# Optimization experiments

Measured on AMD Instinct MI355X. Metric: run time of the kernel, lower is better.

The kernel has to match this reference:

```python
import jax, jax.numpy as jnp
import numpy as np

B, S, D, H = 2, 2048, 1280, 16
DEPTH = D // H  # 80


def setup_inputs() -> dict:
    key = jax.random.key(0)
    ks = jax.random.split(key, 6)
    scale = 1.0 / np.sqrt(D)
    x = jax.random.normal(ks[0], (B, S, D), dtype=jnp.float32)
    # causal mask: 1.0 where attention is disallowed (strict upper triangle)
    mask = jnp.triu(jnp.ones((S, S), dtype=jnp.float32), k=1)
    Wq = jax.random.normal(ks[1], (D, D), dtype=jnp.float32) * scale
    Wk = jax.random.normal(ks[2], (D, D), dtype=jnp.float32) * scale
    Wv = jax.random.normal(ks[3], (D, D), dtype=jnp.float32) * scale
    Wo = jax.random.normal(ks[4], (D, D), dtype=jnp.float32) * scale
    z = jnp.zeros((D,), dtype=jnp.float32)
    return {"x": x, "mask": mask, "Wq": Wq, "bq": z, "Wk": Wk, "bk": z,
            "Wv": Wv, "bv": z, "Wo": Wo, "bo": z}


def _split_heads(t):
    # [B, S, D] -> [B, H, S, depth]
    return t.reshape(B, -1, H, DEPTH).transpose(0, 2, 1, 3)


def reference(x, mask, Wq, bq, Wk, bk, Wv, bv, Wo, bo):
    q = _split_heads(x @ Wq + bq)
    k = _split_heads(x @ Wk + bk)
    v = _split_heads(x @ Wv + bv)
    # scaled dot-product attention with additive (masked * -10000) logits
    logits = jnp.einsum("bhqd,bhkd->bhqk", q, k) / jnp.sqrt(
        jnp.asarray(DEPTH, dtype=jnp.float32))
    logits = logits + mask * -10000.0  # mask broadcasts over [B, H]
    attn = jax.nn.softmax(logits, axis=-1)
    ctx = jnp.einsum("bhqk,bhkd->bhqd", attn, v)
    ctx = ctx.transpose(0, 2, 1, 3).reshape(B, -1, D)  # merge heads
    return ctx @ Wo + bo
```

## Files before the change

### kernel.cpp

```cpp
#include <hip/hip_runtime.h>

typedef unsigned short u16;
typedef __bf16 bf16;
typedef __bf16 bf16x8 __attribute__((ext_vector_type(8)));
typedef unsigned short u16x8 __attribute__((ext_vector_type(8)));
typedef float f32x4 __attribute__((ext_vector_type(4)));

constexpr int B_ = 2, S_ = 2048, D_ = 1280, H_ = 16, DEPTH_ = 80;
constexpr int M_ = B_ * S_;
constexpr int QR_ = 128;

__device__ inline u16 f2b(float f) { return __builtin_bit_cast(u16, (bf16)f); }

typedef __attribute__((address_space(1))) const void gvoid;
typedef __attribute__((address_space(3))) void lvoid;
__device__ inline void gl_lds16(const void* g, void* l) {
  __builtin_amdgcn_global_load_lds((gvoid*)g, (lvoid*)l, 16, 0, 0);
}

__global__ __launch_bounds__(256) void convx_k(const float* __restrict__ src,
                                               u16* __restrict__ dst) {
  int i0 = (blockIdx.x * 256 + threadIdx.x) * 8;
  u16x8 v;
#pragma unroll
  for (int j = 0; j < 8; ++j) v[j] = f2b(src[i0 + j]);
  *(u16x8*)(dst + i0) = v;
}

__global__ __launch_bounds__(256) void pad0_k(u16* __restrict__ QK) {
  int c = blockIdx.x * 256 + threadIdx.x;
  int r = c / 6, k = c - r * 6;
  u16x8 z = {};
  *(u16x8*)(QK + (size_t)r * QR_ + 80 + k * 8) = z;
}

__global__ __launch_bounds__(256) void transpose4_k(const float* W0, const float* W1,
                                                    const float* W2, const float* W3,
                                                    u16* __restrict__ WT) {
  const float* srcs[4] = {W0, W1, W2, W3};
  const float* W = srcs[blockIdx.z];
  u16* out = WT + (size_t)blockIdx.z * D_ * D_;
  __shared__ u16 t[32][33];
  int tx = threadIdx.x, ty = threadIdx.y;
  int x0 = blockIdx.x * 32, y0 = blockIdx.y * 32;
#pragma unroll
  for (int i = 0; i < 4; ++i)
    t[ty + 8 * i][tx] = f2b(W[(size_t)(y0 + ty + 8 * i) * D_ + x0 + tx]);
  __syncthreads();
#pragma unroll
  for (int i = 0; i < 4; ++i)
    out[(size_t)(x0 + ty + 8 * i) * D_ + y0 + tx] = t[tx][ty + 8 * i];
}

struct GemmAcc {
  f32x4 acc[4][4];
};
__device__ inline void gemm_core(const u16* __restrict__ A,
                                 const u16* __restrict__ BT, int m0, int n0,
                                 u16* a_s, u16* b_s, GemmAcc& g) {
  int tid = threadIdx.x, lane = tid & 63, wave = tid >> 6;
  int quad = lane >> 4, l15 = lane & 15;
  int wm = wave >> 1, wn = wave & 1;
  int rr8 = lane >> 3;
  int csw = ((lane & 7) ^ rr8) * 8;
  int sw15 = l15 & 7;

  for (int k0 = 0; k0 < D_; k0 += 64) {
    __syncthreads();
#pragma unroll
    for (int j = 0; j < 4; ++j) {
      int ch = wave * 4 + j;
      gl_lds16(A + (size_t)(m0 + ch * 8 + rr8) * D_ + k0 + csw, a_s + ch * 512);
      gl_lds16(BT + (size_t)(n0 + ch * 8 + rr8) * D_ + k0 + csw, b_s + ch * 512);
    }
    __syncthreads();
#pragma unroll
    for (int ks = 0; ks < 2; ++ks) {
      int pos = (((ks << 2) | quad) ^ sw15) * 8;
      bf16x8 af[4], bfr[4];
#pragma unroll
      for (int mt = 0; mt < 4; ++mt)
        af[mt] = *(const bf16x8*)(a_s + (wm * 64 + mt * 16 + l15) * 64 + pos);
#pragma unroll
      for (int nt = 0; nt < 4; ++nt)
        bfr[nt] = *(const bf16x8*)(b_s + (wn * 64 + nt * 16 + l15) * 64 + pos);
#pragma unroll
      for (int mt = 0; mt < 4; ++mt)
#pragma unroll
        for (int nt = 0; nt < 4; ++nt)
          g.acc[mt][nt] = __builtin_amdgcn_mfma_f32_16x16x32_bf16(
              af[mt], bfr[nt], g.acc[mt][nt], 0, 0, 0);
    }
  }
}

__global__ __launch_bounds__(256) void gemm_qkv(const u16* __restrict__ A,
                                                const u16* __restrict__ BT,
                                                const float* __restrict__ bq,
                                                const float* __restrict__ bk,
                                                const float* __restrict__ bv,
                                                u16* __restrict__ Qw,
                                                u16* __restrict__ Kw,
                                                u16* __restrict__ Vw) {
  __shared__ __align__(16) u16 a_s[128 * 64];
  __shared__ __align__(16) u16 b_s[128 * 64];
  int lane = threadIdx.x & 63, wave = threadIdx.x >> 6;
  int quad = lane >> 4, l15 = lane & 15;
  int wm = wave >> 1, wn = wave & 1;
  int m0 = blockIdx.y * 128, n0 = blockIdx.x * 128;

  GemmAcc g = {};
  gemm_core(A, BT, m0, n0, a_s, b_s, g);

  int mat = n0 / D_;
  const float* bp = (mat == 0) ? bq : (mat == 1 ? bk : bv);
#pragma unroll
  for (int nt = 0; nt < 4; ++nt) {
    int ng = n0 + wn * 64 + nt * 16 + l15;
    int co = ng - mat * D_;
    float bv_ = bp[co];
    int h = co / DEPTH_, d = co % DEPTH_;
#pragma unroll
    for (int mt = 0; mt < 4; ++mt)
#pragma unroll
      for (int r = 0; r < 4; ++r) {
        int row = m0 + wm * 64 + mt * 16 + quad * 4 + r;
        int b = row >> 11, s = row & (S_ - 1);
        u16 bits = f2b(g.acc[mt][nt][r] + bv_);
        if (mat < 2) {
          u16* outp = mat ? Kw : Qw;
          outp[((size_t)(b * H_ + h) * S_ + s) * QR_ + d] = bits;
        } else {
          Vw[((size_t)(b * H_ + h) * DEPTH_ + d) * S_ + s] = bits;
        }
      }
  }
}

__global__ __launch_bounds__(256) void gemm_out(const u16* __restrict__ A,
                                                const u16* __restrict__ BT,
                                                const float* __restrict__ bias,
                                                float* __restrict__ out) {
  __shared__ __align__(16) u16 a_s[128 * 64];
  __shared__ __align__(16) u16 b_s[128 * 64];
  int lane = threadIdx.x & 63, wave = threadIdx.x >> 6;
  int quad = lane >> 4, l15 = lane & 15;
  int wm = wave >> 1, wn = wave & 1;
  int m0 = blockIdx.y * 128, n0 = blockIdx.x * 128;

  GemmAcc g = {};
  gemm_core(A, BT, m0, n0, a_s, b_s, g);

#pragma unroll
  for (int nt = 0; nt < 4; ++nt) {
    int col = n0 + wn * 64 + nt * 16 + l15;
    float bv = bias[col];
#pragma unroll
    for (int mt = 0; mt < 4; ++mt)
#pragma unroll
      for (int r = 0; r < 4; ++r) {
        int row = m0 + wm * 64 + mt * 16 + quad * 4 + r;
        out[(size_t)row * D_ + col] = g.acc[mt][nt][r] + bv;
      }
  }
}

__global__ __launch_bounds__(256, 4) void attn_k(const u16* __restrict__ Qp,
                                                 const u16* __restrict__ Kp,
                                                 const u16* __restrict__ VT,
                                                 u16* __restrict__ ctx) {
  constexpr float SCALE = 0.11180339887498949f;
  __shared__ __align__(16) u16 k_s[64 * 128];
  __shared__ __align__(16) u16 vt_s[80 * 64];
  __shared__ __align__(16) u16 p_s[64 * 72];
  int tid = threadIdx.x, lane = tid & 63, wave = tid >> 6;
  int quad = lane >> 4, l15 = lane & 15;
  int bx = blockIdx.x, by = blockIdx.y;
  int s_ = (by >> 4) & 1;
  int qt = s_ ? (31 - bx) : bx;
  int bh = (by & 15) | (((by >> 5) & 1) << 4);
  const u16* Qb = Qp + (size_t)bh * S_ * QR_;
  const u16* Kb = Kp + (size_t)bh * S_ * QR_;
  const u16* Vb = VT + (size_t)bh * DEPTH_ * S_;

  bf16x8 qf[3];
#pragma unroll
  for (int ks = 0; ks < 3; ++ks)
    qf[ks] = *(const bf16x8*)(Qb + (size_t)(qt * 64 + wave * 16 + l15) * QR_ +
                              ks * 32 + quad * 8);

  f32x4 acc_o[5] = {};
  float lsum[4] = {};

  for (int kt = 0; kt <= qt; ++kt) {
    int k0 = kt * 64;
    __syncthreads();
#pragma unroll
    for (int i = 0; i < 4; ++i) {
      int row = wave * 4 + quad + 16 * i;
      int sc = l15 ^ (row & 7);
      gl_lds16(Kb + (size_t)(k0 + row) * QR_ + sc * 8,
               k_s + (size_t)row * QR_ + l15 * 8);
    }
#pragma unroll
    for (int i = 0; i < 3; ++i) {
      int ch = tid + 256 * i;
      if (ch < 640) {
        int row = ch >> 3, pos = ch & 7;
        int sc = pos ^ (row & 7);
        gl_lds16(Vb + (size_t)row * S_ + k0 + sc * 8, vt_s + ch * 8);
      }
    }
    __syncthreads();

    f32x4 sa[4] = {};
#pragma unroll
    for (int ks = 0; ks < 3; ++ks) {
      int pa = ((ks * 4 + quad) ^ (l15 & 7)) * 8;
#pragma unroll
      for (int nt = 0; nt < 4; ++nt) {
        bf16x8 bfr = *(const bf16x8*)(k_s + (size_t)(nt * 16 + l15) * QR_ + pa);
        sa[nt] = __builtin_amdgcn_mfma_f32_16x16x32_bf16(qf[ks], bfr, sa[nt], 0, 0, 0);
      }
    }
    bool diag = (kt == qt);
#pragma unroll
    for (int nt = 0; nt < 4; ++nt)
#pragma unroll
      for (int r = 0; r < 4; ++r) {
        float p = __expf(sa[nt][r] * SCALE);
        if (diag && (nt * 16 + l15) > (wave * 16 + quad * 4 + r)) p = 0.0f;
        sa[nt][r] = p;
        lsum[r] += p;
      }
    asm volatile("s_waitcnt lgkmcnt(0)" ::: "memory");
#pragma unroll
    for (int nt = 0; nt < 4; ++nt)
#pragma unroll
      for (int r = 0; r < 4; ++r)
        p_s[(wave * 16 + quad * 4 + r) * 72 + nt * 16 + l15] = f2b(sa[nt][r]);
    asm volatile("s_waitcnt lgkmcnt(0)" ::: "memory");
#pragma unroll
    for (int kk = 0; kk < 2; ++kk) {
      bf16x8 af = *(const bf16x8*)(p_s + (wave * 16 + l15) * 72 + kk * 32 + quad * 8);
#pragma unroll
      for (int d5 = 0; d5 < 5; ++d5) {
        int pv = ((kk * 4 + quad) ^ (l15 & 7)) * 8;
        bf16x8 bfr = *(const bf16x8*)(vt_s + (size_t)(d5 * 16 + l15) * 64 + pv);
        acc_o[d5] = __builtin_amdgcn_mfma_f32_16x16x32_bf16(af, bfr, acc_o[d5], 0, 0, 0);
      }
    }
  }

#pragma unroll
  for (int r = 0; r < 4; ++r)
#pragma unroll
    for (int m = 1; m < 16; m <<= 1) lsum[r] += __shfl_xor(lsum[r], m, 16);

  int b = bh >> 4, h = bh & 15;
#pragma unroll
  for (int d5 = 0; d5 < 5; ++d5)
#pragma unroll
    for (int r = 0; r < 4; ++r) {
      int s = qt * 64 + wave * 16 + quad * 4 + r;
      int col = h * DEPTH_ + d5 * 16 + l15;
      ctx[(size_t)(b * S_ + s) * D_ + col] = f2b(acc_o[d5][r] / lsum[r]);
    }
}

extern "C" void kernel_launch(void* const* d_in, const int* in_sizes, int n_in,
                              void* d_out, int out_size, void* d_ws, size_t ws_size,
                              hipStream_t stream) {
  const float* x  = (const float*)d_in[0];
  const float* Wq = (const float*)d_in[2];
  const float* bq = (const float*)d_in[3];
  const float* Wk = (const float*)d_in[4];
  const float* bk = (const float*)d_in[5];
  const float* Wv = (const float*)d_in[6];
  const float* bv = (const float*)d_in[7];
  const float* Wo = (const float*)d_in[8];
  const float* bo = (const float*)d_in[9];

  const size_t DD = (size_t)D_ * D_;
  const size_t QE = (size_t)B_ * H_ * S_ * DEPTH_;
  const size_t QP = (size_t)B_ * H_ * S_ * QR_;
  u16* xbf = (u16*)d_ws;
  u16* wT  = xbf + QE;
  u16* Qw  = wT + 4 * DD;
  u16* Kw  = Qw + QP;
  u16* Vw  = Kw + QP;
  u16* Cw  = xbf;
  size_t need = (size_t)(Vw + QE - xbf) * 2;
  if (ws_size < need) return;

  convx_k<<<(int)(QE / 2048), 256, 0, stream>>>(x, xbf);
  pad0_k<<<3072, 256, 0, stream>>>(Qw);
  transpose4_k<<<dim3(D_ / 32, D_ / 32, 4), dim3(32, 8), 0, stream>>>(Wq, Wk, Wv,
                                                                      Wo, wT);
  gemm_qkv<<<dim3(3 * D_ / 128, M_ / 128), 256, 0, stream>>>(xbf, wT, bq, bk, bv,
                                                             Qw, Kw, Vw);
  attn_k<<<dim3(16, 64), 256, 0, stream>>>(Qw, Kw, Vw, Cw);
  gemm_out<<<dim3(D_ / 128, M_ / 128), 256, 0, stream>>>(Cw, wT + 3 * DD, bo,
                                                         (float*)d_out);
}
```

Baseline: 276.1 us.

## Merge prep kernels into one launch and shrink GEMM K-tile to 32

Folds the x conversion, Q/K padding zeroing and the four weight transposes into a single prep kernel, cutting two launches. The shared GEMM core moves from a 64-wide K tile with XOR-swizzled LDS to a 32-wide unswizzled tile, halving LDS per block. Launch bounds are raised to 4 blocks per CU to allow higher occupancy. The price is twice as many barrier-separated K iterations and possible LDS bank conflicts from dropping the swizzle.

```diff
diff --git a/kernel.cpp b/kernel.cpp
--- a/kernel.cpp
+++ b/kernel.cpp
@@ -18,38 +18,43 @@
   __builtin_amdgcn_global_load_lds((gvoid*)g, (lvoid*)l, 16, 0, 0);
 }
 
-__global__ __launch_bounds__(256) void convx_k(const float* __restrict__ src,
-                                               u16* __restrict__ dst) {
-  int i0 = (blockIdx.x * 256 + threadIdx.x) * 8;
-  u16x8 v;
-#pragma unroll
-  for (int j = 0; j < 8; ++j) v[j] = f2b(src[i0 + j]);
-  *(u16x8*)(dst + i0) = v;
-}
-
-__global__ __launch_bounds__(256) void pad0_k(u16* __restrict__ QK) {
-  int c = blockIdx.x * 256 + threadIdx.x;
-  int r = c / 6, k = c - r * 6;
-  u16x8 z = {};
-  *(u16x8*)(QK + (size_t)r * QR_ + 80 + k * 8) = z;
-}
-
-__global__ __launch_bounds__(256) void transpose4_k(const float* W0, const float* W1,
-                                                    const float* W2, const float* W3,
-                                                    u16* __restrict__ WT) {
-  const float* srcs[4] = {W0, W1, W2, W3};
-  const float* W = srcs[blockIdx.z];
-  u16* out = WT + (size_t)blockIdx.z * D_ * D_;
+__global__ __launch_bounds__(256) void prep_k(const float* __restrict__ x,
+                                              u16* __restrict__ xbf,
+                                              u16* __restrict__ QK,
+                                              const float* __restrict__ W0,
+                                              const float* __restrict__ W1,
+                                              const float* __restrict__ W2,
+                                              const float* __restrict__ W3,
+                                              u16* __restrict__ WT) {
   __shared__ u16 t[32][33];
-  int tx = threadIdx.x, ty = threadIdx.y;
-  int x0 = blockIdx.x * 32, y0 = blockIdx.y * 32;
-#pragma unroll
-  for (int i = 0; i < 4; ++i)
-    t[ty + 8 * i][tx] = f2b(W[(size_t)(y0 + ty + 8 * i) * D_ + x0 + tx]);
-  __syncthreads();
-#pragma unroll
-  for (int i = 0; i < 4; ++i)
-    out[(size_t)(x0 + ty + 8 * i) * D_ + y0 + tx] = t[tx][ty + 8 * i];
+  int bid = blockIdx.x, tid = threadIdx.x;
+  if (bid < 2560) {
+    int i0 = (bid * 256 + tid) * 8;
+    u16x8 v;
+#pragma unroll
+    for (int j = 0; j < 8; ++j) v[j] = f2b(x[i0 + j]);
+    *(u16x8*)(xbf + i0) = v;
+  } else if (bid < 5632) {
+    int c = (bid - 2560) * 256 + tid;
+    int r = c / 6, k = c - r * 6;
+    u16x8 z = {};
+    *(u16x8*)(QK + (size_t)r * QR_ + 80 + k * 8) = z;
+  } else {
+    int tt = bid - 5632;
+    int z = tt / 1600, w = tt - z * 1600;
+    int x0 = (w % 40) * 32, y0 = (w / 40) * 32;
+    const float* srcs[4] = {W0, W1, W2, W3};
+    const float* W = srcs[z];
+    u16* out = WT + (size_t)z * D_ * D_;
+    int tx = tid & 31, ty = tid >> 5;
+#pragma unroll
+    for (int i = 0; i < 4; ++i)
+      t[ty + 8 * i][tx] = f2b(W[(size_t)(y0 + ty + 8 * i) * D_ + x0 + tx]);
+    __syncthreads();
+#pragma unroll
+    for (int i = 0; i < 4; ++i)
+      out[(size_t)(x0 + ty + 8 * i) * D_ + y0 + tx] = t[tx][ty + 8 * i];
+  }
 }
 
 struct GemmAcc {
@@ -61,49 +66,43 @@
   int tid = threadIdx.x, lane = tid & 63, wave = tid >> 6;
   int quad = lane >> 4, l15 = lane & 15;
   int wm = wave >> 1, wn = wave & 1;
-  int rr8 = lane >> 3;
-  int csw = ((lane & 7) ^ rr8) * 8;
-  int sw15 = l15 & 7;
-
-  for (int k0 = 0; k0 < D_; k0 += 64) {
-    __syncthreads();
-#pragma unroll
-    for (int j = 0; j < 4; ++j) {
-      int ch = wave * 4 + j;
-      gl_lds16(A + (size_t)(m0 + ch * 8 + rr8) * D_ + k0 + csw, a_s + ch * 512);
-      gl_lds16(BT + (size_t)(n0 + ch * 8 + rr8) * D_ + k0 + csw, b_s + ch * 512);
-    }
-    __syncthreads();
-#pragma unroll
-    for (int ks = 0; ks < 2; ++ks) {
-      int pos = (((ks << 2) | quad) ^ sw15) * 8;
-      bf16x8 af[4], bfr[4];
-#pragma unroll
-      for (int mt = 0; mt < 4; ++mt)
-        af[mt] = *(const bf16x8*)(a_s + (wm * 64 + mt * 16 + l15) * 64 + pos);
+  int r4 = lane >> 2, c4 = (lane & 3) * 8;
+
+  for (int k0 = 0; k0 < D_; k0 += 32) {
+    __syncthreads();
+#pragma unroll
+    for (int j = 0; j < 2; ++j) {
+      int ch = wave * 2 + j;
+      gl_lds16(A + (size_t)(m0 + ch * 16 + r4) * D_ + k0 + c4, a_s + ch * 512);
+      gl_lds16(BT + (size_t)(n0 + ch * 16 + r4) * D_ + k0 + c4, b_s + ch * 512);
+    }
+    __syncthreads();
+    bf16x8 af[4], bfr[4];
+#pragma unroll
+    for (int mt = 0; mt < 4; ++mt)
+      af[mt] = *(const bf16x8*)(a_s + (wm * 64 + mt * 16 + l15) * 32 + quad * 8);
+#pragma unroll
+    for (int nt = 0; nt < 4; ++nt)
+      bfr[nt] = *(const bf16x8*)(b_s + (wn * 64 + nt * 16 + l15) * 32 + quad * 8);
+#pragma unroll
+    for (int mt = 0; mt < 4; ++mt)
 #pragma unroll
       for (int nt = 0; nt < 4; ++nt)
-        bfr[nt] = *(const bf16x8*)(b_s + (wn * 64 + nt * 16 + l15) * 64 + pos);
-#pragma unroll
-      for (int mt = 0; mt < 4; ++mt)
-#pragma unroll
-        for (int nt = 0; nt < 4; ++nt)
-          g.acc[mt][nt] = __builtin_amdgcn_mfma_f32_16x16x32_bf16(
-              af[mt], bfr[nt], g.acc[mt][nt], 0, 0, 0);
-    }
-  }
-}
-
-__global__ __launch_bounds__(256) void gemm_qkv(const u16* __restrict__ A,
-                                                const u16* __restrict__ BT,
-                                                const float* __restrict__ bq,
-                                                const float* __restrict__ bk,
-                                                const float* __restrict__ bv,
-                                                u16* __restrict__ Qw,
-                                                u16* __restrict__ Kw,
-                                                u16* __restrict__ Vw) {
-  __shared__ __align__(16) u16 a_s[128 * 64];
-  __shared__ __align__(16) u16 b_s[128 * 64];
+        g.acc[mt][nt] = __builtin_amdgcn_mfma_f32_16x16x32_bf16(
+            af[mt], bfr[nt], g.acc[mt][nt], 0, 0, 0);
+  }
+}
+
+__global__ __launch_bounds__(256, 4) void gemm_qkv(const u16* __restrict__ A,
+                                                   const u16* __restrict__ BT,
+                                                   const float* __restrict__ bq,
+                                                   const float* __restrict__ bk,
+                                                   const float* __restrict__ bv,
+                                                   u16* __restrict__ Qw,
+                                                   u16* __restrict__ Kw,
+                                                   u16* __restrict__ Vw) {
+  __shared__ __align__(16) u16 a_s[128 * 32];
+  __shared__ __align__(16) u16 b_s[128 * 32];
   int lane = threadIdx.x & 63, wave = threadIdx.x >> 6;
   int quad = lane >> 4, l15 = lane & 15;
   int wm = wave >> 1, wn = wave & 1;
@@ -137,12 +136,12 @@
   }
 }
 
-__global__ __launch_bounds__(256) void gemm_out(const u16* __restrict__ A,
-                                                const u16* __restrict__ BT,
-                                                const float* __restrict__ bias,
-                                                float* __restrict__ out) {
-  __shared__ __align__(16) u16 a_s[128 * 64];
-  __shared__ __align__(16) u16 b_s[128 * 64];
+__global__ __launch_bounds__(256, 4) void gemm_out(const u16* __restrict__ A,
+                                                   const u16* __restrict__ BT,
+                                                   const float* __restrict__ bias,
+                                                   float* __restrict__ out) {
+  __shared__ __align__(16) u16 a_s[128 * 32];
+  __shared__ __align__(16) u16 b_s[128 * 32];
   int lane = threadIdx.x & 63, wave = threadIdx.x >> 6;
   int quad = lane >> 4, l15 = lane & 15;
   int wm = wave >> 1, wn = wave & 1;
@@ -293,10 +292,7 @@
   size_t need = (size_t)(Vw + QE - xbf) * 2;
   if (ws_size < need) return;
 
-  convx_k<<<(int)(QE / 2048), 256, 0, stream>>>(x, xbf);
-  pad0_k<<<3072, 256, 0, stream>>>(Qw);
-  transpose4_k<<<dim3(D_ / 32, D_ / 32, 4), dim3(32, 8), 0, stream>>>(Wq, Wk, Wv,
-                                                                      Wo, wT);
+  prep_k<<<12032, 256, 0, stream>>>(x, xbf, Qw, Wq, Wk, Wv, Wo, wT);
   gemm_qkv<<<dim3(3 * D_ / 128, M_ / 128), 256, 0, stream>>>(xbf, wT, bq, bk, bv,
                                                              Qw, Kw, Vw);
   attn_k<<<dim3(16, 64), 256, 0, stream>>>(Qw, Kw, Vw, Cw);
```

New measurement: 274.2 us. About the same (-0.7%).
